# Optimization experiments

Measured on AMD Instinct MI355X. Metric: run time of the kernel, lower is better.

The kernel has to match this reference:

```python
import jax, jax.numpy as jnp
import numpy as np

D, B, L, E, H, F = 6, 4, 2048, 1024, 16, 4096
DH = E // H
DECAY = 16.0
CSCALE = 1.0
EPS = 1e-5


def _ln(x, w, b):
    m = jnp.mean(x, axis=-1, keepdims=True)
    v = jnp.mean(jnp.square(x - m), axis=-1, keepdims=True)
    return (x - m) * jax.lax.rsqrt(v + EPS) * w + b


def setup_inputs() -> dict:
    key = jax.random.key(0)
    ks = jax.random.split(key, 10)
    s = 0.02
    f32 = jnp.float32
    return {
        "x": jax.random.normal(ks[0], (B, L, E), f32),
        "Wq": jax.random.normal(ks[1], (D, E, E), f32) * s,
        "Wk": jax.random.normal(ks[2], (D, E, E), f32) * s,
        "bq": jnp.zeros((D, E), f32),
        "bk": jnp.zeros((D, E), f32),
        "ln1_w": jnp.ones((D, E), f32), "ln1_b": jnp.zeros((D, E), f32),
        "ln2_w": jnp.ones((D, E), f32), "ln2_b": jnp.zeros((D, E), f32),
        "ln3_w": jnp.ones((D, E), f32), "ln3_b": jnp.zeros((D, E), f32),
        "W1": jax.random.normal(ks[3], (D, F, E), f32) * s,
        "b1": jnp.zeros((D, F), f32),
        "W2": jax.random.normal(ks[4], (D, E, F), f32) * s,
        "b2": jnp.zeros((D, E), f32),
    }


def reference(x, Wq, Wk, bq, bk, ln1_w, ln1_b, ln2_w, ln2_b, ln3_w, ln3_b, W1, b1, W2, b2):
    seq = x.shape[1]
    pos = jnp.arange(seq)
    # exponential relative-position bias exp(-|i-j|/decay), shared by all layers
    rel = jnp.exp(-jnp.abs(pos[:, None] - pos[None, :]).astype(x.dtype) / DECAY)
    inv_sqrt_d = 1.0 / np.sqrt(DH)

    def layer(h, p):
        (wq, wk, bq_, bk_, l1w, l1b, l2w, l2b, l3w, l3b, w1, b1_, w2, b2_) = p
        bh, sl, _ = h.shape
        q = (h @ wq.T + bq_).reshape(bh, sl, H, DH)
        k = (h @ wk.T + bk_).reshape(bh, sl, H, DH)
        scores = jnp.einsum('blhd,bmhd->bhlm', q, k) * inv_sqrt_d
        # torch MHA need_weights=True averages softmax weights over heads
        w_avg = jax.nn.softmax(scores, axis=-1).mean(axis=1)  # [B,L,L]
        new_w = jax.nn.softmax(CSCALE * w_avg + rel[None], axis=-1)
        sa = jnp.einsum('blm,bme->ble', new_w, h)  # value = raw residual stream
        h1 = _ln(h + sa, l1w, l1b)
        h2 = _ln(h1, l2w, l2b)  # Noop cross-attn block (LayerNorm scale-invariant)
        ff = jax.nn.relu(h2 @ w1.T + b1_) @ w2.T + b2_
        return _ln(h2 + ff, l3w, l3b), None

    out, _ = jax.lax.scan(layer, x, (Wq, Wk, bq, bk, ln1_w, ln1_b, ln2_w, ln2_b,
                                     ln3_w, ln3_b, W1, b1, W2, b2))
    return out
```

## Files before the change

### kernel.cpp

```cpp
#include <hip/hip_runtime.h>

#define D_ 6
#define B_ 4
#define L_ 2048
#define E_ 1024
#define H_ 16
#define F_ 4096
#define BL_ (B_ * L_)
#define QKS 2048
#define EPS_ 1e-5f

typedef __bf16 bf16x8 __attribute__((ext_vector_type(8)));
typedef __bf16 bf16x4 __attribute__((ext_vector_type(4)));
typedef float f32x4 __attribute__((ext_vector_type(4)));

__device__ __forceinline__ void gload_lds16(const void* g, void* l) {
  __builtin_amdgcn_global_load_lds(
      (const __attribute__((address_space(1))) void*)g,
      (__attribute__((address_space(3))) void*)l, 16, 0, 0);
}

__device__ __forceinline__ void stage_tile64(__bf16* ldsb,
                                             const __bf16* gbase, long ldg,
                                             int tid) {
#pragma unroll
  for (int j = 0; j < 2; ++j) {
    int unit = j * 256 + tid;
    int row = unit >> 3, cu = unit & 7;
    const __bf16* src = gbase + (long)row * ldg + ((cu ^ (row & 7)) << 3);
    gload_lds16(src, ldsb + (long)((j * 256 + (tid & ~63)) << 3));
  }
}

#define RD_FRAG(ldsb, r_, kk) \
  (*(const bf16x8*)&(ldsb)[((r_) * 8 + (((kk) * 4 + l4) ^ ((r_) & 7))) * 8])

#define LDA_SUB(P, MH)                                                        \
  _Pragma("unroll") for (int mi = 0; mi < 4; ++mi)                            \
  _Pragma("unroll") for (int kk = 0; kk < 2; ++kk) {                          \
    int r_ = wr + (MH) * 64 + mi * 16 + l15;                                  \
    int cu_ = kk * 4 + l4;                                                    \
    aF[mi][kk] = *(const bf16x8*)&lds[P][0][(r_ * 8 + (cu_ ^ (r_ & 7))) * 8]; \
  }

#define LDB_SUB(P, BF, NH)                                                    \
  _Pragma("unroll") for (int ni = 0; ni < 2; ++ni)                            \
  _Pragma("unroll") for (int kk = 0; kk < 2; ++kk) {                          \
    int r_ = wc + (NH) * 32 + ni * 16 + l15;                                  \
    int cu_ = kk * 4 + l4;                                                    \
    BF[ni][kk] = *(const bf16x8*)&lds[P][1][(r_ * 8 + (cu_ ^ (r_ & 7))) * 8]; \
  }

#define MFMA_Q(AF, BF, MH, NH)                                                \
  _Pragma("unroll") for (int mi = 0; mi < 4; ++mi)                            \
  _Pragma("unroll") for (int ni = 0; ni < 2; ++ni)                            \
  _Pragma("unroll") for (int kk = 0; kk < 2; ++kk)                            \
    acc[(MH) * 4 + mi][(NH) * 2 + ni] =                                       \
        __builtin_amdgcn_mfma_f32_16x16x32_bf16(                              \
            AF[mi][kk], BF[ni][kk], acc[(MH) * 4 + mi][(NH) * 2 + ni], 0, 0, 0);

#define PHASE_PRE()                                                           \
  __builtin_amdgcn_s_barrier();                                               \
  asm volatile("s_waitcnt lgkmcnt(0)" ::: "memory");                          \
  __builtin_amdgcn_sched_barrier(0);                                          \
  __builtin_amdgcn_s_setprio(1)

#define PHASE_POST()                                                          \
  __builtin_amdgcn_s_setprio(0);                                              \
  __builtin_amdgcn_sched_barrier(0);                                          \
  __builtin_amdgcn_s_barrier()

template <int EPI>
__global__ __launch_bounds__(512, 2) void gemm8p(
    const __bf16* __restrict__ A, const __bf16* __restrict__ Bm,
    float* __restrict__ Cf, __bf16* __restrict__ Cb,
    const float* __restrict__ bias, int M, int N, int K, int lda, int ldb,
    int zk, long strA, long strB, long strC, long strCk) {
  __shared__ __bf16 lds[2][2][256 * 64];
  const int tid = threadIdx.x;
  const int wave = tid >> 6, lane = tid & 63;
  const int l15 = lane & 15, l4 = lane >> 4;
  const int z = blockIdx.y;
  const int kc = (zk == 2) ? (z & 1) : 0;
  const int bat = (zk == 2) ? (z >> 1) : z;
  const __bf16* Ab = A + (long)bat * strA + (long)kc * K;
  const __bf16* Bb = Bm + (long)bat * strB + (long)kc * K;
  const long coff = (long)bat * strC + (long)kc * strCk;

  const int nbx = N >> 8;
  const int nwg = (M >> 8) * nbx;
  const int orig = blockIdx.x;
  const int qq = nwg >> 3, rr = nwg & 7;
  const int xcd = orig & 7, lid = orig >> 3;
  const int wg = (xcd < rr ? xcd * (qq + 1) : rr * (qq + 1) + (xcd - rr) * qq) + lid;
  const int row0 = (wg / nbx) * 256, col0 = (wg % nbx) * 256;
  const int wr = (wave >> 2) * 128;
  const int wc = (wave & 3) * 64;

  auto STAGE = [&](int bufi, int mat, int hf, const __bf16* Gp, int ldm,
                   int grow0, int k0) {
#pragma unroll
    for (int j = 0; j < 2; ++j) {
      int rowh = j * 64 + (tid >> 3);
      int row = hf * 128 + rowh;
      const __bf16* src =
          Gp + (long)(grow0 + row) * ldm + k0 + (((lane & 7) ^ (lane >> 3)) << 3);
      __bf16* dst = &lds[bufi][mat][(hf * 1024 + j * 512 + wave * 64) * 8];
      gload_lds16(src, dst);
    }
  };

  const int NT = K >> 6;
  STAGE(0, 0, 0, Ab, lda, row0, 0);
  STAGE(0, 0, 1, Ab, lda, row0, 0);
  STAGE(0, 1, 0, Bb, ldb, col0, 0);
  STAGE(0, 1, 1, Bb, ldb, col0, 0);
  STAGE(1, 0, 0, Ab, lda, row0, 64);
  STAGE(1, 1, 0, Bb, ldb, col0, 64);
  STAGE(1, 0, 1, Ab, lda, row0, 64);
  asm volatile("s_waitcnt vmcnt(6)" ::: "memory");
  __builtin_amdgcn_s_barrier();

  f32x4 acc[8][4];
#pragma unroll
  for (int i = 0; i < 8; ++i)
#pragma unroll
    for (int j = 0; j < 4; ++j) acc[i][j] = (f32x4){0.f, 0.f, 0.f, 0.f};
  bf16x8 aF[4][2], b0F[2][2], b1F[2][2];

  for (int t = 0; t < NT; ++t) {
    const int p = t & 1;
    const int kA = (t + 1 < NT ? t + 1 : NT - 1) << 6;
    const int kB = (t + 2 < NT ? t + 2 : NT - 1) << 6;
    LDA_SUB(p, 0);
    LDB_SUB(p, b0F, 0);
    STAGE(p ^ 1, 1, 1, Bb, ldb, col0, kA);
    PHASE_PRE();
    MFMA_Q(aF, b0F, 0, 0);
    PHASE_POST();
    LDB_SUB(p, b1F, 1);
    PHASE_PRE();
    MFMA_Q(aF, b1F, 0, 1);
    PHASE_POST();
    LDA_SUB(p, 1);
    STAGE(p, 1, 0, Bb, ldb, col0, kB);
    PHASE_PRE();
    MFMA_Q(aF, b0F, 1, 0);
    PHASE_POST();
    STAGE(p, 0, 0, Ab, lda, row0, kB);
    STAGE(p, 0, 1, Ab, lda, row0, kB);
    __builtin_amdgcn_s_barrier();
    __builtin_amdgcn_sched_barrier(0);
    __builtin_amdgcn_s_setprio(1);
    MFMA_Q(aF, b1F, 1, 1);
    __builtin_amdgcn_s_setprio(0);
    __builtin_amdgcn_sched_barrier(0);
    asm volatile("s_waitcnt vmcnt(6)" ::: "memory");
    __builtin_amdgcn_s_barrier();
  }
  asm volatile("s_waitcnt vmcnt(0)" ::: "memory");

#pragma unroll
  for (int i = 0; i < 8; ++i) {
    int row = row0 + wr + (i >> 2) * 64 + (i & 3) * 16 + l4 * 4;
#pragma unroll
    for (int j = 0; j < 4; ++j) {
      int col = col0 + wc + (j >> 1) * 32 + (j & 1) * 16 + l15;
      float bval = 0.f;
      if constexpr (EPI == 1 || EPI == 2) bval = bias[col];
#pragma unroll
      for (int r = 0; r < 4; ++r) {
        long crow = row + r;
        float v = acc[i][j][r];
        if constexpr (EPI == 1 || EPI == 2) v += bval;
        if constexpr (EPI == 2) v = fmaxf(v, 0.f);
        long ci = coff + crow * N + col;
        if constexpr (EPI == 1 || EPI == 2)
          Cb[ci] = (__bf16)v;
        else
          Cf[ci] = v;
      }
    }
  }
}

__global__ __launch_bounds__(256, 2) void attn_stats_kernel(
    const __bf16* __restrict__ qk, float* __restrict__ sinv) {
  __shared__ __bf16 sQ[64 * 64];
  __shared__ __bf16 sK[2][64 * 64];
  const int tid = threadIdx.x, wave = tid >> 6, lane = tid & 63;
  const int l15 = lane & 15, l4 = lane >> 4;
  const int l0 = blockIdx.x * 64, h = blockIdx.y, b = blockIdx.z;
  const __bf16* Qb = qk + ((long)(b * L_ + l0)) * QKS + h * 64;
  const __bf16* Kb = qk + ((long)b * L_) * QKS + 1024 + h * 64;

  stage_tile64(sQ, Qb, QKS, tid);
  stage_tile64(sK[0], Kb, QKS, tid);
  asm volatile("s_waitcnt vmcnt(0)" ::: "memory");
  __builtin_amdgcn_s_barrier();

  const int rA = wave * 16 + l15;
  const bf16x8 aF0 = RD_FRAG(sQ, rA, 0);
  const bf16x8 aF1 = RD_FRAG(sQ, rA, 1);

  float msum[4] = {0.f, 0.f, 0.f, 0.f};
  int p = 0;
  for (int m0 = 0; m0 < 32; ++m0) {
    const int mn = (m0 + 1 < 32) ? m0 + 1 : 31;
    stage_tile64(sK[p ^ 1], Kb + (long)mn * 64 * QKS, QKS, tid);
    asm volatile("s_waitcnt vmcnt(2)" ::: "memory");
    __builtin_amdgcn_s_barrier();
#pragma unroll
    for (int ni = 0; ni < 4; ++ni) {
      const int rB = ni * 16 + l15;
      bf16x8 b0 = RD_FRAG(sK[p], rB, 0);
      bf16x8 b1 = RD_FRAG(sK[p], rB, 1);
      f32x4 s = (f32x4){0.f, 0.f, 0.f, 0.f};
      s = __builtin_amdgcn_mfma_f32_16x16x32_bf16(aF0, b0, s, 0, 0, 0);
      s = __builtin_amdgcn_mfma_f32_16x16x32_bf16(aF1, b1, s, 0, 0, 0);
#pragma unroll
      for (int r = 0; r < 4; ++r) msum[r] += __expf(s[r] * 0.125f);
    }
    asm volatile("" ::: "memory");
    __builtin_amdgcn_s_barrier();
    p ^= 1;
  }
#pragma unroll
  for (int r = 0; r < 4; ++r) {
    float s = msum[r];
    for (int d = 1; d < 16; d <<= 1) s += __shfl_xor(s, d, 64);
    if (l15 == 0) {
      long idx = ((long)(b * H_ + h)) * L_ + l0 + wave * 16 + l4 * 4 + r;
      sinv[idx] = 1.0f / s;
    }
  }
}

__global__ __launch_bounds__(256, 2) void attn_probs_kernel(
    const __bf16* __restrict__ qk, const float* __restrict__ sinv,
    __bf16* __restrict__ P) {
  __shared__ __bf16 sT[2][2][64 * 64];
  const int tid = threadIdx.x, wave = tid >> 6, lane = tid & 63;
  const int l15 = lane & 15, l4 = lane >> 4;
  const int m0 = blockIdx.x * 64, l0 = blockIdx.y * 64, b = blockIdx.z;
  const __bf16* Qb = qk + ((long)(b * L_ + l0)) * QKS;
  const __bf16* Kb = qk + ((long)(b * L_ + m0)) * QKS + 1024;

  stage_tile64(sT[0][0], Qb, QKS, tid);
  stage_tile64(sT[0][1], Kb, QKS, tid);

  float wacc[4][4];
#pragma unroll
  for (int i = 0; i < 4; ++i)
#pragma unroll
    for (int j = 0; j < 4; ++j) wacc[i][j] = 0.f;

  const int rA = wave * 16 + l15;
  int p = 0;
  for (int h = 0; h < H_; ++h) {
    const int hn = (h + 1 < H_) ? h + 1 : H_ - 1;
    stage_tile64(sT[p ^ 1][0], Qb + hn * 64, QKS, tid);
    stage_tile64(sT[p ^ 1][1], Kb + hn * 64, QKS, tid);
    float iv[4];
#pragma unroll
    for (int r = 0; r < 4; ++r) {
      long idx = ((long)(b * H_ + h)) * L_ + l0 + wave * 16 + l4 * 4 + r;
      iv[r] = sinv[idx];
    }
    asm volatile("s_waitcnt vmcnt(4)" ::: "memory");
    __builtin_amdgcn_s_barrier();
    bf16x8 aF0 = RD_FRAG(sT[p][0], rA, 0);
    bf16x8 aF1 = RD_FRAG(sT[p][0], rA, 1);
#pragma unroll
    for (int ni = 0; ni < 4; ++ni) {
      const int rB = ni * 16 + l15;
      bf16x8 b0 = RD_FRAG(sT[p][1], rB, 0);
      bf16x8 b1 = RD_FRAG(sT[p][1], rB, 1);
      f32x4 s = (f32x4){0.f, 0.f, 0.f, 0.f};
      s = __builtin_amdgcn_mfma_f32_16x16x32_bf16(aF0, b0, s, 0, 0, 0);
      s = __builtin_amdgcn_mfma_f32_16x16x32_bf16(aF1, b1, s, 0, 0, 0);
#pragma unroll
      for (int r = 0; r < 4; ++r)
        wacc[ni][r] += __expf(s[r] * 0.125f) * iv[r];
    }
    asm volatile("" ::: "memory");
    __builtin_amdgcn_s_barrier();
    p ^= 1;
  }
#pragma unroll
  for (int ni = 0; ni < 4; ++ni) {
#pragma unroll
    for (int r = 0; r < 4; ++r) {
      int row = l0 + wave * 16 + l4 * 4 + r;
      int col = m0 + ni * 16 + l15;
      float rel = __expf(-fabsf((float)(row - col)) * (1.0f / 16.0f));
      float t = wacc[ni][r] * (1.0f / H_) + rel;
      P[((long)b * L_ + row) * L_ + col] = (__bf16)__expf(t);
    }
  }
}

__global__ __launch_bounds__(256, 4) void rowinv_kernel(
    const __bf16* __restrict__ P, float* __restrict__ rowinv) {
  const long row = blockIdx.x;
  const __bf16* p = P + row * (long)L_;
  bf16x8 v = *(const bf16x8*)&p[threadIdx.x * 8];
  float s = 0.f;
#pragma unroll
  for (int j = 0; j < 8; ++j) s += (float)v[j];
  for (int d = 1; d < 64; d <<= 1) s += __shfl_xor(s, d, 64);
  __shared__ float sh[4];
  if ((threadIdx.x & 63) == 0) sh[threadIdx.x >> 6] = s;
  __syncthreads();
  if (threadIdx.x == 0) rowinv[row] = 1.0f / (sh[0] + sh[1] + sh[2] + sh[3]);
}

__device__ __forceinline__ void wave_reduce2(float& a, float& b) {
#pragma unroll
  for (int d = 1; d < 64; d <<= 1) {
    a += __shfl_xor(a, d, 64);
    b += __shfl_xor(b, d, 64);
  }
}

__global__ __launch_bounds__(256, 4) void ln12_kernel(
    const float* __restrict__ hin, const float* __restrict__ p0,
    const float* __restrict__ p1, const float* __restrict__ rowinv,
    const float* __restrict__ w1, const float* __restrict__ b1,
    const float* __restrict__ w2, const float* __restrict__ b2,
    float* __restrict__ h2f, __bf16* __restrict__ h2b) {
  __shared__ float sh[8];
  const int tid = threadIdx.x;
  const long row = blockIdx.x;
  const long base = row * E_ + tid * 4;
  const float rinv = rowinv[row];
  f32x4 hv = *(const f32x4*)&hin[base];
  f32x4 p0v = *(const f32x4*)&p0[base];
  f32x4 p1v = *(const f32x4*)&p1[base];
  float y[4];
  float s1 = 0.f, s2 = 0.f;
#pragma unroll
  for (int j = 0; j < 4; ++j) {
    y[j] = hv[j] + rinv * (p0v[j] + p1v[j]);
    s1 += y[j];
    s2 += y[j] * y[j];
  }
  wave_reduce2(s1, s2);
  if ((tid & 63) == 0) { sh[(tid >> 6) * 2] = s1; sh[(tid >> 6) * 2 + 1] = s2; }
  __syncthreads();
  s1 = sh[0] + sh[2] + sh[4] + sh[6];
  s2 = sh[1] + sh[3] + sh[5] + sh[7];
  float mean = s1 * (1.f / E_);
  float var = s2 * (1.f / E_) - mean * mean;
  float rs = rsqrtf(var + EPS_);
  f32x4 wv = *(const f32x4*)&w1[tid * 4];
  f32x4 bv = *(const f32x4*)&b1[tid * 4];
  float h1[4];
  s1 = 0.f; s2 = 0.f;
#pragma unroll
  for (int j = 0; j < 4; ++j) {
    h1[j] = (y[j] - mean) * rs * wv[j] + bv[j];
    s1 += h1[j];
    s2 += h1[j] * h1[j];
  }
  __syncthreads();
  wave_reduce2(s1, s2);
  if ((tid & 63) == 0) { sh[(tid >> 6) * 2] = s1; sh[(tid >> 6) * 2 + 1] = s2; }
  __syncthreads();
  s1 = sh[0] + sh[2] + sh[4] + sh[6];
  s2 = sh[1] + sh[3] + sh[5] + sh[7];
  mean = s1 * (1.f / E_);
  var = s2 * (1.f / E_) - mean * mean;
  rs = rsqrtf(var + EPS_);
  wv = *(const f32x4*)&w2[tid * 4];
  bv = *(const f32x4*)&b2[tid * 4];
  f32x4 o;
  bf16x4 ob;
#pragma unroll
  for (int j = 0; j < 4; ++j) {
    float v = (h1[j] - mean) * rs * wv[j] + bv[j];
    o[j] = v;
    ob[j] = (__bf16)v;
  }
  *(f32x4*)&h2f[base] = o;
  *(bf16x4*)&h2b[base] = ob;
}

__global__ __launch_bounds__(256, 4) void ln3_kernel(
    const float* __restrict__ h2f, const float* __restrict__ p0,
    const float* __restrict__ p1, const float* __restrict__ bias2,
    const float* __restrict__ w3, const float* __restrict__ b3,
    float* __restrict__ outf, __bf16* __restrict__ outb) {
  __shared__ float sh[8];
  const int tid = threadIdx.x;
  const long row = blockIdx.x;
  const long base = row * E_ + tid * 4;
  f32x4 hv = *(const f32x4*)&h2f[base];
  f32x4 p0v = *(const f32x4*)&p0[base];
  f32x4 p1v = *(const f32x4*)&p1[base];
  f32x4 b2v = *(const f32x4*)&bias2[tid * 4];
  float y[4];
  float s1 = 0.f, s2 = 0.f;
#pragma unroll
  for (int j = 0; j < 4; ++j) {
    y[j] = hv[j] + p0v[j] + p1v[j] + b2v[j];
    s1 += y[j];
    s2 += y[j] * y[j];
  }
  wave_reduce2(s1, s2);
  if ((tid & 63) == 0) { sh[(tid >> 6) * 2] = s1; sh[(tid >> 6) * 2 + 1] = s2; }
  __syncthreads();
  s1 = sh[0] + sh[2] + sh[4] + sh[6];
  s2 = sh[1] + sh[3] + sh[5] + sh[7];
  float mean = s1 * (1.f / E_);
  float var = s2 * (1.f / E_) - mean * mean;
  float rs = rsqrtf(var + EPS_);
  f32x4 wv = *(const f32x4*)&w3[tid * 4];
  f32x4 bv = *(const f32x4*)&b3[tid * 4];
  f32x4 o;
  bf16x4 ob;
#pragma unroll
  for (int j = 0; j < 4; ++j) {
    float v = (y[j] - mean) * rs * wv[j] + bv[j];
    o[j] = v;
    ob[j] = (__bf16)v;
  }
  *(f32x4*)&outf[base] = o;
  *(bf16x4*)&outb[base] = ob;
}

__global__ __launch_bounds__(256, 4) void transpose_kernel(
    const __bf16* __restrict__ X, __bf16* __restrict__ XT) {
  __shared__ __bf16 t[64 * 66];
  const int l0 = blockIdx.x * 64, e0 = blockIdx.y * 64, b = blockIdx.z;
  const int tid = threadIdx.x;
#pragma unroll
  for (int r = 0; r < 2; ++r) {
    int c = tid + 256 * r;
    int rw = c >> 3, c8 = (c & 7) * 8;
    *(bf16x8*)&t[rw * 66 + c8] =
        *(const bf16x8*)&X[((long)(b * L_) + l0 + rw) * E_ + e0 + c8];
  }
  __syncthreads();
#pragma unroll
  for (int r = 0; r < 2; ++r) {
    int c = tid + 256 * r;
    int er = c >> 3, l8 = (c & 7) * 8;
    bf16x8 v;
#pragma unroll
    for (int j = 0; j < 8; ++j) v[j] = t[(l8 + j) * 66 + er];
    *(bf16x8*)&XT[((long)(b * E_) + e0 + er) * L_ + l0 + l8] = v;
  }
}

__global__ __launch_bounds__(256, 4) void f32_to_bf16_kernel(
    const float* __restrict__ x, __bf16* __restrict__ y) {
  long i = ((long)blockIdx.x * 256 + threadIdx.x) * 4;
  f32x4 v = *(const f32x4*)&x[i];
  bf16x4 o;
#pragma unroll
  for (int j = 0; j < 4; ++j) o[j] = (__bf16)v[j];
  *(bf16x4*)&y[i] = o;
}

__global__ __launch_bounds__(256, 4) void build_wqk_kernel(
    const float* __restrict__ Wq, const float* __restrict__ Wk,
    __bf16* __restrict__ out) {
  long i = ((long)blockIdx.x * 256 + threadIdx.x) * 4;
  long d = i >> 21;
  long rem = i & ((1L << 21) - 1);
  long row = rem >> 10, col = rem & 1023;
  const float* src = (row < 1024)
                         ? &Wq[(d << 20) + (row << 10) + col]
                         : &Wk[(d << 20) + ((row - 1024) << 10) + col];
  f32x4 v = *(const f32x4*)src;
  bf16x4 o;
#pragma unroll
  for (int j = 0; j < 4; ++j) o[j] = (__bf16)v[j];
  *(bf16x4*)&out[i] = o;
}

__global__ __launch_bounds__(256, 4) void build_bqk_kernel(
    const float* __restrict__ bq, const float* __restrict__ bk,
    float* __restrict__ out) {
  int i = blockIdx.x * 256 + threadIdx.x;
  int d = i >> 11, c = i & 2047;
  out[i] = (c < 1024) ? bq[d * 1024 + c] : bk[d * 1024 + c - 1024];
}

extern "C" void kernel_launch(void* const* d_in, const int* in_sizes, int n_in,
                              void* d_out, int out_size, void* d_ws,
                              size_t ws_size, hipStream_t stream) {
  const float* x = (const float*)d_in[0];
  const float* Wq = (const float*)d_in[1];
  const float* Wk = (const float*)d_in[2];
  const float* bq = (const float*)d_in[3];
  const float* bk = (const float*)d_in[4];
  const float* l1w = (const float*)d_in[5];
  const float* l1b = (const float*)d_in[6];
  const float* l2w = (const float*)d_in[7];
  const float* l2b = (const float*)d_in[8];
  const float* l3w = (const float*)d_in[9];
  const float* l3b = (const float*)d_in[10];
  const float* W1 = (const float*)d_in[11];
  const float* b1 = (const float*)d_in[12];
  const float* W2 = (const float*)d_in[13];
  const float* b2 = (const float*)d_in[14];

  char* p = (char*)d_ws;
  auto take = [&](size_t bytes) -> char* {
    char* r = p;
    p += (bytes + 255) & ~(size_t)255;
    return r;
  };
  __bf16* wqk_bf = (__bf16*)take((size_t)D_ * 2048 * 1024 * 2);
  __bf16* w1_bf = (__bf16*)take((size_t)D_ * F_ * E_ * 2);
  __bf16* w2_bf = (__bf16*)take((size_t)D_ * E_ * F_ * 2);
  __bf16* h_bf = (__bf16*)take((size_t)BL_ * E_ * 2);
  __bf16* hT = (__bf16*)take((size_t)BL_ * E_ * 2);
  __bf16* qk_bf = (__bf16*)take((size_t)BL_ * QKS * 2);
  __bf16* Pbuf = (__bf16*)take((size_t)B_ * L_ * L_ * 2);
  __bf16* ffmid = qk_bf;
  float* bqk = (float*)take((size_t)D_ * 2048 * 4);
  float* sinv = (float*)take((size_t)B_ * H_ * L_ * 4);
  float* rowinv = (float*)take((size_t)B_ * L_ * 4);
  float* part = (float*)take((size_t)2 * BL_ * E_ * 4);
  float* part0 = part;
  float* part1 = part + (size_t)BL_ * E_;
  float* hbuf = (float*)take((size_t)BL_ * E_ * 4);

  build_wqk_kernel<<<D_ * 2048 * 1024 / 1024, 256, 0, stream>>>(Wq, Wk, wqk_bf);
  build_bqk_kernel<<<D_ * 2048 / 256, 256, 0, stream>>>(bq, bk, bqk);
  f32_to_bf16_kernel<<<D_ * F_ * E_ / 1024, 256, 0, stream>>>(W1, w1_bf);
  f32_to_bf16_kernel<<<D_ * E_ * F_ / 1024, 256, 0, stream>>>(W2, w2_bf);
  f32_to_bf16_kernel<<<BL_ * E_ / 1024, 256, 0, stream>>>(x, h_bf);
  transpose_kernel<<<dim3(L_ / 64, E_ / 64, B_), 256, 0, stream>>>(h_bf, hT);

  const float* h_in = x;
  for (int d = 0; d < D_; ++d) {
    gemm8p<1><<<dim3(256, 1), 512, 0, stream>>>(
        h_bf, wqk_bf + (size_t)d * 2048 * 1024, nullptr, qk_bf,
        bqk + d * 2048, BL_, 2048, E_, E_, E_, 1, 0, 0, 0, 0);
    attn_stats_kernel<<<dim3(L_ / 64, H_, B_), 256, 0, stream>>>(qk_bf, sinv);
    attn_probs_kernel<<<dim3(L_ / 64, L_ / 64, B_), 256, 0, stream>>>(
        qk_bf, sinv, Pbuf);
    rowinv_kernel<<<B_ * L_, 256, 0, stream>>>(Pbuf, rowinv);
    gemm8p<0><<<dim3(32, 8), 512, 0, stream>>>(
        Pbuf, hT, part, nullptr, nullptr, L_, E_, L_ / 2, L_, L_, 2,
        (long)L_ * L_, (long)E_ * L_, (long)L_ * E_, (long)BL_ * E_);
    ln12_kernel<<<BL_, 256, 0, stream>>>(h_in, part0, part1, rowinv,
                                         l1w + d * E_, l1b + d * E_,
                                         l2w + d * E_, l2b + d * E_, hbuf,
                                         h_bf);
    gemm8p<2><<<dim3(512, 1), 512, 0, stream>>>(
        h_bf, w1_bf + (size_t)d * F_ * E_, nullptr, ffmid, b1 + d * F_, BL_,
        F_, E_, E_, E_, 1, 0, 0, 0, 0);
    gemm8p<0><<<dim3(128, 2), 512, 0, stream>>>(
        ffmid, w2_bf + (size_t)d * E_ * F_, part, nullptr, nullptr, BL_, E_,
        F_ / 2, F_, F_, 2, 0, 0, 0, (long)BL_ * E_);
    float* outp = (d == D_ - 1) ? (float*)d_out : hbuf;
    ln3_kernel<<<BL_, 256, 0, stream>>>(hbuf, part0, part1, b2 + d * E_,
                                        l3w + d * E_, l3b + d * E_, outp,
                                        h_bf);
    if (d < D_ - 1) {
      transpose_kernel<<<dim3(L_ / 64, E_ / 64, B_), 256, 0, stream>>>(h_bf, hT);
      h_in = hbuf;
    }
  }
}
```

Before: 2.526 ms.

## Fuse row-sum into probs kernel, store split-K partials in bf16, precompute stage pointers

The attention-probs kernel now writes per-64-column partial row sums, which removes the separate rowinv pass that re-read the full LxL probability matrix. The LN kernels reduce those 32 partials themselves. The split-K GEMM partials are written as bf16 instead of f32, halving their write and read traffic, at some cost in precision on the residual sums. GEMM staging now uses source pointers computed once instead of recomputing addresses in a lambda on every stage.

```diff
diff --git a/kernel.cpp b/kernel.cpp
--- a/kernel.cpp
+++ b/kernel.cpp
@@ -70,12 +70,28 @@
   __builtin_amdgcn_sched_barrier(0);                                          \
   __builtin_amdgcn_s_barrier()
 
+#define STAGE_A(BUFI, HF, K0)                                                 \
+  do {                                                                        \
+    gload_lds16(sA[HF][0] + (K0),                                             \
+                &lds[BUFI][0][((HF) * 1024 + wave * 64) * 8]);                \
+    gload_lds16(sA[HF][1] + (K0),                                             \
+                &lds[BUFI][0][((HF) * 1024 + 512 + wave * 64) * 8]);          \
+  } while (0)
+
+#define STAGE_B(BUFI, HF, K0)                                                 \
+  do {                                                                        \
+    gload_lds16(sB[HF][0] + (K0),                                             \
+                &lds[BUFI][1][((HF) * 1024 + wave * 64) * 8]);                \
+    gload_lds16(sB[HF][1] + (K0),                                             \
+                &lds[BUFI][1][((HF) * 1024 + 512 + wave * 64) * 8]);          \
+  } while (0)
+
 template <int EPI>
 __global__ __launch_bounds__(512, 2) void gemm8p(
     const __bf16* __restrict__ A, const __bf16* __restrict__ Bm,
-    float* __restrict__ Cf, __bf16* __restrict__ Cb,
-    const float* __restrict__ bias, int M, int N, int K, int lda, int ldb,
-    int zk, long strA, long strB, long strC, long strCk) {
+    __bf16* __restrict__ Cb, const float* __restrict__ bias, int M, int N,
+    int K, int lda, int ldb, int zk, long strA, long strB, long strC,
+    long strCk) {
   __shared__ __bf16 lds[2][2][256 * 64];
   const int tid = threadIdx.x;
   const int wave = tid >> 6, lane = tid & 63;
@@ -97,27 +113,26 @@
   const int wr = (wave >> 2) * 128;
   const int wc = (wave & 3) * 64;
 
-  auto STAGE = [&](int bufi, int mat, int hf, const __bf16* Gp, int ldm,
-                   int grow0, int k0) {
+  const int rsel = tid >> 3;
+  const int swz = ((lane & 7) ^ (rsel & 7)) << 3;
+  const __bf16* sA[2][2];
+  const __bf16* sB[2][2];
+#pragma unroll
+  for (int hf = 0; hf < 2; ++hf)
 #pragma unroll
     for (int j = 0; j < 2; ++j) {
-      int rowh = j * 64 + (tid >> 3);
-      int row = hf * 128 + rowh;
-      const __bf16* src =
-          Gp + (long)(grow0 + row) * ldm + k0 + (((lane & 7) ^ (lane >> 3)) << 3);
-      __bf16* dst = &lds[bufi][mat][(hf * 1024 + j * 512 + wave * 64) * 8];
-      gload_lds16(src, dst);
-    }
-  };
+      sA[hf][j] = Ab + (long)(row0 + hf * 128 + j * 64 + rsel) * lda + swz;
+      sB[hf][j] = Bb + (long)(col0 + hf * 128 + j * 64 + rsel) * ldb + swz;
+    }
 
   const int NT = K >> 6;
-  STAGE(0, 0, 0, Ab, lda, row0, 0);
-  STAGE(0, 0, 1, Ab, lda, row0, 0);
-  STAGE(0, 1, 0, Bb, ldb, col0, 0);
-  STAGE(0, 1, 1, Bb, ldb, col0, 0);
-  STAGE(1, 0, 0, Ab, lda, row0, 64);
-  STAGE(1, 1, 0, Bb, ldb, col0, 64);
-  STAGE(1, 0, 1, Ab, lda, row0, 64);
+  STAGE_A(0, 0, 0);
+  STAGE_A(0, 1, 0);
+  STAGE_B(0, 0, 0);
+  STAGE_B(0, 1, 0);
+  STAGE_A(1, 0, 64);
+  STAGE_B(1, 0, 64);
+  STAGE_A(1, 1, 64);
   asm volatile("s_waitcnt vmcnt(6)" ::: "memory");
   __builtin_amdgcn_s_barrier();
 
@@ -134,7 +149,7 @@
     const int kB = (t + 2 < NT ? t + 2 : NT - 1) << 6;
     LDA_SUB(p, 0);
     LDB_SUB(p, b0F, 0);
-    STAGE(p ^ 1, 1, 1, Bb, ldb, col0, kA);
+    STAGE_B(p ^ 1, 1, kA);
     PHASE_PRE();
     MFMA_Q(aF, b0F, 0, 0);
     PHASE_POST();
@@ -143,12 +158,12 @@
     MFMA_Q(aF, b1F, 0, 1);
     PHASE_POST();
     LDA_SUB(p, 1);
-    STAGE(p, 1, 0, Bb, ldb, col0, kB);
+    STAGE_B(p, 0, kB);
     PHASE_PRE();
     MFMA_Q(aF, b0F, 1, 0);
     PHASE_POST();
-    STAGE(p, 0, 0, Ab, lda, row0, kB);
-    STAGE(p, 0, 1, Ab, lda, row0, kB);
+    STAGE_A(p, 0, kB);
+    STAGE_A(p, 1, kB);
     __builtin_amdgcn_s_barrier();
     __builtin_amdgcn_sched_barrier(0);
     __builtin_amdgcn_s_setprio(1);
@@ -174,11 +189,7 @@
         float v = acc[i][j][r];
         if constexpr (EPI == 1 || EPI == 2) v += bval;
         if constexpr (EPI == 2) v = fmaxf(v, 0.f);
-        long ci = coff + crow * N + col;
-        if constexpr (EPI == 1 || EPI == 2)
-          Cb[ci] = (__bf16)v;
-        else
-          Cf[ci] = v;
+        Cb[coff + crow * N + col] = (__bf16)v;
       }
     }
   }
@@ -238,7 +249,7 @@
 
 __global__ __launch_bounds__(256, 2) void attn_probs_kernel(
     const __bf16* __restrict__ qk, const float* __restrict__ sinv,
-    __bf16* __restrict__ P) {
+    __bf16* __restrict__ P, float* __restrict__ rowsumT) {
   __shared__ __bf16 sT[2][2][64 * 64];
   const int tid = threadIdx.x, wave = tid >> 6, lane = tid & 63;
   const int l15 = lane & 15, l4 = lane >> 4;
@@ -287,6 +298,7 @@
     __builtin_amdgcn_s_barrier();
     p ^= 1;
   }
+  float rowpart[4] = {0.f, 0.f, 0.f, 0.f};
 #pragma unroll
   for (int ni = 0; ni < 4; ++ni) {
 #pragma unroll
@@ -294,25 +306,23 @@
       int row = l0 + wave * 16 + l4 * 4 + r;
       int col = m0 + ni * 16 + l15;
       float rel = __expf(-fabsf((float)(row - col)) * (1.0f / 16.0f));
-      float t = wacc[ni][r] * (1.0f / H_) + rel;
-      P[((long)b * L_ + row) * L_ + col] = (__bf16)__expf(t);
-    }
-  }
-}
-
-__global__ __launch_bounds__(256, 4) void rowinv_kernel(
-    const __bf16* __restrict__ P, float* __restrict__ rowinv) {
-  const long row = blockIdx.x;
-  const __bf16* p = P + row * (long)L_;
-  bf16x8 v = *(const bf16x8*)&p[threadIdx.x * 8];
-  float s = 0.f;
-#pragma unroll
-  for (int j = 0; j < 8; ++j) s += (float)v[j];
-  for (int d = 1; d < 64; d <<= 1) s += __shfl_xor(s, d, 64);
-  __shared__ float sh[4];
-  if ((threadIdx.x & 63) == 0) sh[threadIdx.x >> 6] = s;
-  __syncthreads();
-  if (threadIdx.x == 0) rowinv[row] = 1.0f / (sh[0] + sh[1] + sh[2] + sh[3]);
+      float pv = __expf(wacc[ni][r] * (1.0f / H_) + rel);
+      P[((long)b * L_ + row) * L_ + col] = (__bf16)pv;
+      rowpart[r] += pv;
+    }
+  }
+#pragma unroll
+  for (int r = 0; r < 4; ++r) {
+    float s = rowpart[r];
+    s += __shfl_xor(s, 1, 16);
+    s += __shfl_xor(s, 2, 16);
+    s += __shfl_xor(s, 4, 16);
+    s += __shfl_xor(s, 8, 16);
+    if (l15 == 0) {
+      int row = l0 + wave * 16 + l4 * 4 + r;
+      rowsumT[((long)b * L_ + row) * 32 + (m0 >> 6)] = s;
+    }
+  }
 }
 
 __device__ __forceinline__ void wave_reduce2(float& a, float& b) {
@@ -324,24 +334,31 @@
 }
 
 __global__ __launch_bounds__(256, 4) void ln12_kernel(
-    const float* __restrict__ hin, const float* __restrict__ p0,
-    const float* __restrict__ p1, const float* __restrict__ rowinv,
+    const float* __restrict__ hin, const __bf16* __restrict__ p0,
+    const __bf16* __restrict__ p1, const float* __restrict__ rowsumT,
     const float* __restrict__ w1, const float* __restrict__ b1,
     const float* __restrict__ w2, const float* __restrict__ b2,
     float* __restrict__ h2f, __bf16* __restrict__ h2b) {
-  __shared__ float sh[8];
+  __shared__ float sh[9];
   const int tid = threadIdx.x;
   const long row = blockIdx.x;
   const long base = row * E_ + tid * 4;
-  const float rinv = rowinv[row];
+  if (tid < 32) {
+    float s = rowsumT[row * 32 + tid];
+#pragma unroll
+    for (int d = 1; d < 32; d <<= 1) s += __shfl_xor(s, d, 32);
+    if (tid == 0) sh[8] = s;
+  }
   f32x4 hv = *(const f32x4*)&hin[base];
-  f32x4 p0v = *(const f32x4*)&p0[base];
-  f32x4 p1v = *(const f32x4*)&p1[base];
+  bf16x4 p0v = *(const bf16x4*)&p0[base];
+  bf16x4 p1v = *(const bf16x4*)&p1[base];
+  __syncthreads();
+  const float rinv = 1.0f / sh[8];
   float y[4];
   float s1 = 0.f, s2 = 0.f;
 #pragma unroll
   for (int j = 0; j < 4; ++j) {
-    y[j] = hv[j] + rinv * (p0v[j] + p1v[j]);
+    y[j] = hv[j] + rinv * ((float)p0v[j] + (float)p1v[j]);
     s1 += y[j];
     s2 += y[j] * y[j];
   }
@@ -387,8 +404,8 @@
 }
 
 __global__ __launch_bounds__(256, 4) void ln3_kernel(
-    const float* __restrict__ h2f, const float* __restrict__ p0,
-    const float* __restrict__ p1, const float* __restrict__ bias2,
+    const float* __restrict__ h2f, const __bf16* __restrict__ p0,
+    const __bf16* __restrict__ p1, const float* __restrict__ bias2,
     const float* __restrict__ w3, const float* __restrict__ b3,
     float* __restrict__ outf, __bf16* __restrict__ outb) {
   __shared__ float sh[8];
@@ -396,14 +413,14 @@
   const long row = blockIdx.x;
   const long base = row * E_ + tid * 4;
   f32x4 hv = *(const f32x4*)&h2f[base];
-  f32x4 p0v = *(const f32x4*)&p0[base];
-  f32x4 p1v = *(const f32x4*)&p1[base];
+  bf16x4 p0v = *(const bf16x4*)&p0[base];
+  bf16x4 p1v = *(const bf16x4*)&p1[base];
   f32x4 b2v = *(const f32x4*)&bias2[tid * 4];
   float y[4];
   float s1 = 0.f, s2 = 0.f;
 #pragma unroll
   for (int j = 0; j < 4; ++j) {
-    y[j] = hv[j] + p0v[j] + p1v[j] + b2v[j];
+    y[j] = hv[j] + (float)p0v[j] + (float)p1v[j] + b2v[j];
     s1 += y[j];
     s2 += y[j] * y[j];
   }
@@ -523,10 +540,10 @@
   __bf16* ffmid = qk_bf;
   float* bqk = (float*)take((size_t)D_ * 2048 * 4);
   float* sinv = (float*)take((size_t)B_ * H_ * L_ * 4);
-  float* rowinv = (float*)take((size_t)B_ * L_ * 4);
-  float* part = (float*)take((size_t)2 * BL_ * E_ * 4);
-  float* part0 = part;
-  float* part1 = part + (size_t)BL_ * E_;
+  float* rowsumT = (float*)take((size_t)BL_ * 32 * 4);
+  __bf16* partB = (__bf16*)take((size_t)2 * BL_ * E_ * 2);
+  __bf16* part0 = partB;
+  __bf16* part1 = partB + (size_t)BL_ * E_;
   float* hbuf = (float*)take((size_t)BL_ * E_ * 4);
 
   build_wqk_kernel<<<D_ * 2048 * 1024 / 1024, 256, 0, stream>>>(Wq, Wk, wqk_bf);
@@ -539,25 +556,24 @@
   const float* h_in = x;
   for (int d = 0; d < D_; ++d) {
     gemm8p<1><<<dim3(256, 1), 512, 0, stream>>>(
-        h_bf, wqk_bf + (size_t)d * 2048 * 1024, nullptr, qk_bf,
-        bqk + d * 2048, BL_, 2048, E_, E_, E_, 1, 0, 0, 0, 0);
+        h_bf, wqk_bf + (size_t)d * 2048 * 1024, qk_bf, bqk + d * 2048, BL_,
+        2048, E_, E_, E_, 1, 0, 0, 0, 0);
     attn_stats_kernel<<<dim3(L_ / 64, H_, B_), 256, 0, stream>>>(qk_bf, sinv);
     attn_probs_kernel<<<dim3(L_ / 64, L_ / 64, B_), 256, 0, stream>>>(
-        qk_bf, sinv, Pbuf);
-    rowinv_kernel<<<B_ * L_, 256, 0, stream>>>(Pbuf, rowinv);
+        qk_bf, sinv, Pbuf, rowsumT);
     gemm8p<0><<<dim3(32, 8), 512, 0, stream>>>(
-        Pbuf, hT, part, nullptr, nullptr, L_, E_, L_ / 2, L_, L_, 2,
-        (long)L_ * L_, (long)E_ * L_, (long)L_ * E_, (long)BL_ * E_);
-    ln12_kernel<<<BL_, 256, 0, stream>>>(h_in, part0, part1, rowinv,
+        Pbuf, hT, partB, nullptr, L_, E_, L_ / 2, L_, L_, 2, (long)L_ * L_,
+        (long)E_ * L_, (long)L_ * E_, (long)BL_ * E_);
+    ln12_kernel<<<BL_, 256, 0, stream>>>(h_in, part0, part1, rowsumT,
                                          l1w + d * E_, l1b + d * E_,
                                          l2w + d * E_, l2b + d * E_, hbuf,
                                          h_bf);
     gemm8p<2><<<dim3(512, 1), 512, 0, stream>>>(
-        h_bf, w1_bf + (size_t)d * F_ * E_, nullptr, ffmid, b1 + d * F_, BL_,
-        F_, E_, E_, E_, 1, 0, 0, 0, 0);
+        h_bf, w1_bf + (size_t)d * F_ * E_, ffmid, b1 + d * F_, BL_, F_, E_,
+        E_, E_, 1, 0, 0, 0, 0);
     gemm8p<0><<<dim3(128, 2), 512, 0, stream>>>(
-        ffmid, w2_bf + (size_t)d * E_ * F_, part, nullptr, nullptr, BL_, E_,
-        F_ / 2, F_, F_, 2, 0, 0, 0, (long)BL_ * E_);
+        ffmid, w2_bf + (size_t)d * E_ * F_, partB, nullptr, BL_, E_, F_ / 2,
+        F_, F_, 2, 0, 0, 0, (long)BL_ * E_);
     float* outp = (d == D_ - 1) ? (float*)d_out : hbuf;
     ln3_kernel<<<BL_, 256, 0, stream>>>(hbuf, part0, part1, b2 + d * E_,
                                         l3w + d * E_, l3b + d * E_, outp,
```

Result: faster. 2.412 ms (-4.5%).
